# Kernel tuning notes

Hardware: AMD Instinct MI355X
Metric: run time of the kernel (lower is better)

## Reference

```python
import jax, jax.numpy as jnp
import numpy as np

B, T, C, H = 8, 2048, 768, 64

def setup_inputs() -> dict:
    key = jax.random.key(0)
    k1, k2, k3, k4 = jax.random.split(key, 4)
    x = jax.random.normal(k1, (B, T, C), dtype=jnp.float32)
    Wk = jax.random.normal(k2, (C, H), dtype=jnp.float32) * 0.02
    Wq = jax.random.normal(k3, (C, H), dtype=jnp.float32) * 0.02
    Wv = jax.random.normal(k4, (C, H), dtype=jnp.float32) * 0.02
    return {"x": x, "Wk": Wk, "Wq": Wq, "Wv": Wv}

def reference(x, Wk, Wq, Wv):
    # QKV projections (no bias): [B,T,C] @ [C,H] -> [B,T,H]
    k = jnp.einsum('btc,ch->bth', x, Wk)
    q = jnp.einsum('btc,ch->bth', x, Wq)
    v = jnp.einsum('btc,ch->bth', x, Wv)
    scale = 1.0 / jnp.sqrt(jnp.asarray(q.shape[-1], q.dtype))
    # scores: [B,T,T]
    wei = jnp.einsum('bth,bsh->bts', q, k) * scale
    # causal mask: upper triangle (k=1) set to -inf before softmax
    causal = jnp.tril(jnp.ones((wei.shape[1], wei.shape[2]), dtype=bool))
    wei = jnp.where(causal[None, :, :], wei, -jnp.inf)
    wei = jax.nn.softmax(wei, axis=-1)
    # dropout deterministic (training=False) -> identity
    out = jnp.einsum('bts,bsh->bth', wei, v)
    return out
```

## Files before the change

kernel.cpp:

```cpp
#include <hip/hip_runtime.h>
#include <hip/hip_bf16.h>
#include <stdint.h>

#define BB 8
#define TT 2048
#define CC 768
#define NTPB 72

typedef __bf16 bf16x8 __attribute__((ext_vector_type(8)));
typedef float f32x4 __attribute__((ext_vector_type(4)));
typedef float f32x16 __attribute__((ext_vector_type(16)));

__device__ inline __bf16 f2b(float f) {
    __hip_bfloat16 h = __float2bfloat16(f);
    return __builtin_bit_cast(__bf16, h);
}
__device__ inline ushort f2bits(float f) {
    __hip_bfloat16 h = __float2bfloat16(f);
    return __builtin_bit_cast(ushort, h);
}
__device__ inline float bits2f(ushort u) {
    return __builtin_bit_cast(float, ((uint32_t)u) << 16);
}
__device__ inline uint32_t cvtpk(float lo, float hi) {
    uint32_t r;
    asm("v_cvt_pk_bf16_f32 %0, %1, %2" : "=v"(r) : "v"(lo), "v"(hi));
    return r;
}
__device__ inline void pswap(uint32_t& a, uint32_t& b) {
    asm volatile("v_permlane32_swap_b32 %0, %1" : "+v"(a), "+v"(b));
}

#define GLL16(gp, lp)                                                          \
    __builtin_amdgcn_global_load_lds(                                          \
        (const __attribute__((address_space(1))) unsigned int*)(gp),           \
        (__attribute__((address_space(3))) unsigned int*)(lp), 16, 0, 0)

__launch_bounds__(256)
__global__ void wt_kernel(const float* __restrict__ Wk, const float* __restrict__ Wq,
                          const float* __restrict__ Wv, ushort* __restrict__ WtF) {
    __shared__ float tile[32][65];
    int m  = blockIdx.x / 24;
    int c0 = (blockIdx.x % 24) * 32;
    const float* W = (m == 0) ? Wq : ((m == 1) ? Wk : Wv);
    int tid = threadIdx.x;
    {
        int r   = tid >> 3;
        int col = (tid & 7) * 8;
        float4 v0 = *(const float4*)&W[(size_t)(c0 + r) * 64 + col];
        float4 v1 = *(const float4*)&W[(size_t)(c0 + r) * 64 + col + 4];
        tile[r][col]     = v0.x; tile[r][col + 1] = v0.y;
        tile[r][col + 2] = v0.z; tile[r][col + 3] = v0.w;
        tile[r][col + 4] = v1.x; tile[r][col + 5] = v1.y;
        tile[r][col + 6] = v1.z; tile[r][col + 7] = v1.w;
    }
    __syncthreads();
    int j   = tid >> 2;
    int sub = tid & 3;
    int cc  = sub * 8;
    ushort tmp[8];
#pragma unroll
    for (int e = 0; e < 8; e++) tmp[e] = f2bits(tile[cc + e][j]);
    int kc = c0 >> 5;
    ushort* dst = &WtF[((size_t)kc * 192 + m * 64 + j) * 32 + sub * 8];
    *(uint4*)(dst) = *(uint4*)&tmp[0];
}

__launch_bounds__(256, 3)
__global__ void qkv_kernel(const float* __restrict__ x, const ushort* __restrict__ WtF,
                           ushort* __restrict__ qws, ushort* __restrict__ kws,
                           ushort* __restrict__ vws) {
    __shared__ float  xsA[4][32 * 32];
    __shared__ ushort xsB[3][6144];

    int tid  = threadIdx.x;
    int wid  = tid >> 6;
    int lane = tid & 63;
    int l15  = lane & 15;
    int hi4  = lane >> 4;
    int row0 = blockIdx.x * 32;

    int rA  = tid >> 3;
    int gcA = (tid & 7) ^ (rA & 7);
    const float* gpA = x + (size_t)(row0 + rA) * CC + gcA * 4;

    int PB0 = tid, PB1 = tid + 256, PB2 = tid + 512;
    int LB0 = PB0 ^ ((PB0 >> 3) & 3);
    int LB1 = PB1 ^ ((PB1 >> 3) & 3);
    int LB2 = PB2 ^ ((PB2 >> 3) & 3);

    int PrB[3];
#pragma unroll
    for (int nt = 0; nt < 3; nt++) {
        int Lr = (wid * 48 + nt * 16 + l15) * 4 + hi4;
        PrB[nt] = Lr ^ ((Lr >> 3) & 3);
    }

    f32x4 acc[2][3];
#pragma unroll
    for (int mm = 0; mm < 2; mm++)
#pragma unroll
        for (int nt = 0; nt < 3; nt++) acc[mm][nt] = (f32x4){0.f, 0.f, 0.f, 0.f};

    auto stageA = [&](int t) {
        GLL16(gpA + t * 32, &xsA[t & 3][(size_t)tid * 4]);
    };
    auto stageB = [&](int t) {
        int buf = t % 3;
        const ushort* bsrc = WtF + (size_t)t * 6144;
        GLL16(bsrc + LB0 * 8, &xsB[buf][PB0 * 8]);
        GLL16(bsrc + LB1 * 8, &xsB[buf][PB1 * 8]);
        GLL16(bsrc + LB2 * 8, &xsB[buf][PB2 * 8]);
    };

    stageA(0); stageA(1);
    stageB(0); stageB(1);
    stageA(2); stageA(3);

#pragma unroll
    for (int p = 0; p < 12; p++) {
        if (p < 11) asm volatile("s_waitcnt vmcnt(2)" ::: "memory");
        else        asm volatile("s_waitcnt vmcnt(0)" ::: "memory");
        __builtin_amdgcn_s_barrier();
        __builtin_amdgcn_sched_barrier(0);

#pragma unroll
        for (int u = 0; u < 2; u++) {
            int t    = 2 * p + u;
            int bufA = t & 3;
            int bufB = t % 3;
            bf16x8 af[2];
#pragma unroll
            for (int mm = 0; mm < 2; mm++) {
                int row = mm * 16 + l15;
                const float* base = &xsA[bufA][row * 32];
                float4 fa = *(const float4*)(base + (((2 * hi4)     ^ (row & 7)) * 4));
                float4 fb = *(const float4*)(base + (((2 * hi4 + 1) ^ (row & 7)) * 4));
                uint32_t w0 = cvtpk(fa.x, fa.y), w1 = cvtpk(fa.z, fa.w);
                uint32_t w2 = cvtpk(fb.x, fb.y), w3 = cvtpk(fb.z, fb.w);
                uint4 u4 = {w0, w1, w2, w3};
                af[mm] = __builtin_bit_cast(bf16x8, u4);
            }
#pragma unroll
            for (int nt = 0; nt < 3; nt++) {
                bf16x8 b = __builtin_bit_cast(bf16x8, *(const uint4*)&xsB[bufB][PrB[nt] * 8]);
                acc[0][nt] = __builtin_amdgcn_mfma_f32_16x16x32_bf16(af[0], b, acc[0][nt], 0, 0, 0);
                acc[1][nt] = __builtin_amdgcn_mfma_f32_16x16x32_bf16(af[1], b, acc[1][nt], 0, 0, 0);
            }
        }
        __builtin_amdgcn_s_barrier();
        if (p < 11) { stageB(2 * p + 2); stageB(2 * p + 3); }
        if (p < 10) { stageA(2 * p + 4); stageA(2 * p + 5); }
    }

    const float qscale = 0.125f * 1.4426950408889634f;
    int bidx = row0 >> 11;
#pragma unroll
    for (int mm = 0; mm < 2; mm++) {
        int r0 = row0 + mm * 16 + 4 * hi4;
        int t0 = r0 & 2047;
#pragma unroll
        for (int nt = 0; nt < 3; nt++) {
            int c = wid * 48 + nt * 16 + l15;
            int m = c >> 6;
            int j = c & 63;
            if (m == 0) {
#pragma unroll
                for (int r = 0; r < 4; r++)
                    qws[(size_t)(r0 + r) * 64 + j] = f2bits(acc[mm][nt][r] * qscale);
            } else if (m == 1) {
#pragma unroll
                for (int r = 0; r < 4; r++)
                    kws[(size_t)(r0 + r) * 64 + j] = f2bits(acc[mm][nt][r]);
            } else {
                ushort4 pk;
                pk.x = f2bits(acc[mm][nt][0]);
                pk.y = f2bits(acc[mm][nt][1]);
                pk.z = f2bits(acc[mm][nt][2]);
                pk.w = f2bits(acc[mm][nt][3]);
                *(ushort4*)&vws[((size_t)bidx * 64 + j) * TT + t0] = pk;
            }
        }
    }
}

__launch_bounds__(256, 3)
__global__ void flash_kernel(const ushort* __restrict__ qg, const ushort* __restrict__ kg,
                             const ushort* __restrict__ vtg, float* __restrict__ out,
                             ushort* __restrict__ pO, float* __restrict__ pM,
                             float* __restrict__ pL) {
    __shared__ ushort Ks[3][64 * 64];
    __shared__ ushort Vs[3][64 * 64];

    int tid  = threadIdx.x;
    int wid  = tid >> 6;
    int lane = tid & 63;
    int l31  = lane & 31;
    int hi   = lane >> 5;

    int b  = blockIdx.x & 7;
    int tp = blockIdx.x >> 3;
    int g  = 0;
    while (tp >= ((g + 2) * (g + 2)) >> 2) g++;
    int seg   = tp - (((g + 1) * (g + 1)) >> 2);
    int nseg  = (g + 2) >> 1;
    int Qb    = g * 128;
    int Q0w   = Qb + wid * 32;
    int s_beg = seg * 256;
    int s_end = (s_beg + 256 < Qb + 128) ? s_beg + 256 : Qb + 128;
    int nt    = (s_end - s_beg) >> 6;

    int rS  = tid >> 3;
    int gcS = (tid & 7) ^ (rS & 7);
    const ushort* kS = kg  + ((size_t)b * TT + rS) * 64 + gcS * 8;
    const ushort* vS = vtg + ((size_t)b * 64 + rS) * TT + gcS * 8;

    auto stage = [&](int tt) {
        int buf = tt % 3;
        int ss  = s_beg + tt * 64;
        const ushort* kA = kS + (size_t)ss * 64;
        const ushort* vA = vS + ss;
        GLL16(kA,            &Ks[buf][tid * 8]);
        GLL16(kA + 32 * 64,  &Ks[buf][(tid + 256) * 8]);
        GLL16(vA,            &Vs[buf][tid * 8]);
        GLL16(vA + 32 * TT,  &Vs[buf][(tid + 256) * 8]);
    };

    const ushort* qp = qg + ((size_t)b * TT + Q0w + l31) * 64 + hi * 8;
    bf16x8 qf[4];
#pragma unroll
    for (int c = 0; c < 4; c++)
        qf[c] = __builtin_bit_cast(bf16x8, *(const uint4*)(qp + c * 16));

    f32x16 o0 = (f32x16)(0.f), o1 = (f32x16)(0.f);
    float m  = -INFINITY;
    float lp = 0.f;

    stage(0);
    if (nt > 1) stage(1);

    for (int t = 0; t < nt; t++) {
        if (t < nt - 1) asm volatile("s_waitcnt vmcnt(4)" ::: "memory");
        else            asm volatile("s_waitcnt vmcnt(0)" ::: "memory");
        __builtin_amdgcn_s_barrier();
        __builtin_amdgcn_sched_barrier(0);
        if (t + 2 < nt) stage(t + 2);

        int s0 = s_beg + t * 64;
        if (s0 < Q0w + 32) {
            int buf = t % 3;
            bf16x8 kf[2][4];
#pragma unroll
            for (int tt = 0; tt < 2; tt++) {
                int rk = tt * 32 + l31;
                const ushort* base = &Ks[buf][rk * 64];
                int sw = rk & 7;
#pragma unroll
                for (int c = 0; c < 4; c++)
                    kf[tt][c] = __builtin_bit_cast(bf16x8,
                        *(const uint4*)(base + (((c * 2 + hi) ^ sw) * 8)));
            }

            f32x16 st0 = (f32x16)(0.f), st1 = (f32x16)(0.f);
            __builtin_amdgcn_s_setprio(1);
#pragma unroll
            for (int c = 0; c < 4; c++)
                st0 = __builtin_amdgcn_mfma_f32_32x32x16_bf16(kf[0][c], qf[c], st0, 0, 0, 0);
#pragma unroll
            for (int c = 0; c < 4; c++)
                st1 = __builtin_amdgcn_mfma_f32_32x32x16_bf16(kf[1][c], qf[c], st1, 0, 0, 0);
            __builtin_amdgcn_s_setprio(0);

            if (s0 + 63 > Q0w) {
                int th0 = Q0w + l31 - s0 - 4 * hi;
                int th1 = th0 - 32;
#pragma unroll
                for (int r = 0; r < 16; r++) {
                    int kvl = (r & 3) + 8 * (r >> 2);
                    if (kvl > th0) st0[r] = -INFINITY;
                    if (kvl > th1) st1[r] = -INFINITY;
                }
            }

            float a[16];
#pragma unroll
            for (int r = 0; r < 16; r++) a[r] = fmaxf(st0[r], st1[r]);
#pragma unroll
            for (int off = 8; off > 0; off >>= 1)
#pragma unroll
                for (int i = 0; i < 8; i++)
                    if (i < off) a[i] = fmaxf(a[i], a[i + off]);
            float pmax = fmaxf(a[0], __shfl_xor(a[0], 32));
            if (__any(pmax > m + 11.54f)) {
                float mn = fmaxf(m, pmax);
                float al = exp2f(m - mn);
                lp *= al;
#pragma unroll
                for (int r = 0; r < 16; r++) { o0[r] *= al; o1[r] *= al; }
                m = mn;
            }
#pragma unroll
            for (int r = 0; r < 16; r++) {
                st0[r] = exp2f(st0[r] - m);
                st1[r] = exp2f(st1[r] - m);
            }
            float s[16];
#pragma unroll
            for (int r = 0; r < 16; r++) s[r] = st0[r] + st1[r];
#pragma unroll
            for (int off = 8; off > 0; off >>= 1)
#pragma unroll
                for (int i = 0; i < 8; i++)
                    if (i < off) s[i] += s[i + off];
            lp += s[0];

            bf16x8 pf[4];
            {
                uint32_t w0, w1, w2, w3;
                w0 = cvtpk(st0[0], st0[1]);  w1 = cvtpk(st0[2], st0[3]);
                w2 = cvtpk(st0[4], st0[5]);  w3 = cvtpk(st0[6], st0[7]);
                pswap(w0, w2); pswap(w1, w3);
                uint4 u0 = {w0, w1, w2, w3}; pf[0] = __builtin_bit_cast(bf16x8, u0);
                w0 = cvtpk(st0[8], st0[9]);  w1 = cvtpk(st0[10], st0[11]);
                w2 = cvtpk(st0[12], st0[13]); w3 = cvtpk(st0[14], st0[15]);
                pswap(w0, w2); pswap(w1, w3);
                uint4 u1 = {w0, w1, w2, w3}; pf[1] = __builtin_bit_cast(bf16x8, u1);
                w0 = cvtpk(st1[0], st1[1]);  w1 = cvtpk(st1[2], st1[3]);
                w2 = cvtpk(st1[4], st1[5]);  w3 = cvtpk(st1[6], st1[7]);
                pswap(w0, w2); pswap(w1, w3);
                uint4 u2 = {w0, w1, w2, w3}; pf[2] = __builtin_bit_cast(bf16x8, u2);
                w0 = cvtpk(st1[8], st1[9]);  w1 = cvtpk(st1[10], st1[11]);
                w2 = cvtpk(st1[12], st1[13]); w3 = cvtpk(st1[14], st1[15]);
                pswap(w0, w2); pswap(w1, w3);
                uint4 u3 = {w0, w1, w2, w3}; pf[3] = __builtin_bit_cast(bf16x8, u3);
            }

            bf16x8 vf[2][4];
#pragma unroll
            for (int ht = 0; ht < 2; ht++) {
                int rv = ht * 32 + l31;
                const ushort* base = &Vs[buf][rv * 64];
                int sw = rv & 7;
#pragma unroll
                for (int c = 0; c < 4; c++)
                    vf[ht][c] = __builtin_bit_cast(bf16x8,
                        *(const uint4*)(base + (((c * 2 + hi) ^ sw) * 8)));
            }

            __builtin_amdgcn_s_setprio(1);
#pragma unroll
            for (int c = 0; c < 4; c++)
                o0 = __builtin_amdgcn_mfma_f32_32x32x16_bf16(vf[0][c], pf[c], o0, 0, 0, 0);
#pragma unroll
            for (int c = 0; c < 4; c++)
                o1 = __builtin_amdgcn_mfma_f32_32x32x16_bf16(vf[1][c], pf[c], o1, 0, 0, 0);
            __builtin_amdgcn_s_setprio(0);
        }
    }

    float lsum = lp + __shfl_xor(lp, 32);

    if (nseg == 1) {
        float inv = 1.f / lsum;
        float* ob = out + ((size_t)b * TT + Q0w + l31) * 64;
#pragma unroll
        for (int gg = 0; gg < 4; gg++) {
            float4 v0 = {o0[4*gg] * inv, o0[4*gg+1] * inv, o0[4*gg+2] * inv, o0[4*gg+3] * inv};
            *(float4*)(ob + 8 * gg + 4 * hi) = v0;
            float4 v1 = {o1[4*gg] * inv, o1[4*gg+1] * inv, o1[4*gg+2] * inv, o1[4*gg+3] * inv};
            *(float4*)(ob + 32 + 8 * gg + 4 * hi) = v1;
        }
    } else {
        int tb = b * NTPB + tp;
        ushort* pb = pO + (size_t)tb * 8192 + (size_t)(wid * 32 + l31) * 64;
#pragma unroll
        for (int gg = 0; gg < 4; gg++) {
            ushort4 v0 = {f2bits(o0[4*gg]), f2bits(o0[4*gg+1]),
                          f2bits(o0[4*gg+2]), f2bits(o0[4*gg+3])};
            *(ushort4*)(pb + 8 * gg + 4 * hi) = v0;
            ushort4 v1 = {f2bits(o1[4*gg]), f2bits(o1[4*gg+1]),
                          f2bits(o1[4*gg+2]), f2bits(o1[4*gg+3])};
            *(ushort4*)(pb + 32 + 8 * gg + 4 * hi) = v1;
        }
        if (hi == 0) {
            pM[(size_t)tb * 128 + wid * 32 + l31] = m;
            pL[(size_t)tb * 128 + wid * 32 + l31] = lsum;
        }
    }
}

__launch_bounds__(256)
__global__ void merge_kernel(const ushort* __restrict__ pO, const float* __restrict__ pM,
                             const float* __restrict__ pL, float* __restrict__ out) {
    int b    = blockIdx.x / 56;
    int rem  = blockIdx.x % 56;
    int g    = 2 + (rem >> 2);
    int q4   = rem & 3;
    int nseg = (g + 2) >> 1;
    int tbase = b * NTPB + (((g + 1) * (g + 1)) >> 2);

    int row  = q4 * 32 + (threadIdx.x >> 3);
    int colg = (threadIdx.x & 7) * 8;

    float mstar = -INFINITY;
    for (int s = 0; s < nseg; s++)
        mstar = fmaxf(mstar, pM[(size_t)(tbase + s) * 128 + row]);

    float oa[8] = {0.f, 0.f, 0.f, 0.f, 0.f, 0.f, 0.f, 0.f};
    float la = 0.f;
    for (int s = 0; s < nseg; s++) {
        float w = exp2f(pM[(size_t)(tbase + s) * 128 + row] - mstar);
        la += w * pL[(size_t)(tbase + s) * 128 + row];
        uint4 u = *(const uint4*)&pO[(size_t)(tbase + s) * 8192 + (size_t)row * 64 + colg];
#pragma unroll
        for (int e = 0; e < 4; e++) {
            uint32_t wdw = ((const uint32_t*)&u)[e];
            oa[e*2]     += w * bits2f((ushort)(wdw & 0xffff));
            oa[e*2 + 1] += w * bits2f((ushort)(wdw >> 16));
        }
    }
    float inv = 1.f / la;
    float* ob = out + ((size_t)b * TT + g * 128 + row) * 64 + colg;
    float4 r0 = {oa[0] * inv, oa[1] * inv, oa[2] * inv, oa[3] * inv};
    float4 r1 = {oa[4] * inv, oa[5] * inv, oa[6] * inv, oa[7] * inv};
    *(float4*)(ob)     = r0;
    *(float4*)(ob + 4) = r1;
}

extern "C" void kernel_launch(void* const* d_in, const int* in_sizes, int n_in,
                              void* d_out, int out_size, void* d_ws, size_t ws_size,
                              hipStream_t stream) {
    const float* x  = (const float*)d_in[0];
    const float* Wk = (const float*)d_in[1];
    const float* Wq = (const float*)d_in[2];
    const float* Wv = (const float*)d_in[3];
    float* out = (float*)d_out;

    char* ws = (char*)d_ws;
    ushort* WtF = (ushort*)(ws);
    ushort* qws = (ushort*)(ws + 0x50000);
    ushort* kws = (ushort*)(ws + 0x250000);
    ushort* vws = (ushort*)(ws + 0x450000);
    ushort* pO  = (ushort*)(ws + 0x650000);
    float*  pM  = (float*)(ws + 0x1050000);
    float*  pL  = (float*)(ws + 0x1098000);

    wt_kernel<<<72, 256, 0, stream>>>(Wk, Wq, Wv, WtF);
    qkv_kernel<<<(BB * TT) / 32, 256, 0, stream>>>(x, WtF, qws, kws, vws);
    flash_kernel<<<BB * NTPB, 256, 0, stream>>>(qws, kws, vws, out, pO, pM, pL);
    merge_kernel<<<BB * 14 * 4, 256, 0, stream>>>(pO, pM, pL, out);
}
```

Measured before the change: 45.85 us.

## Split flash attention into 128-key segments for more blocks and higher occupancy

Shortens each flash block's KV segment from up to 256 keys to exactly 128 (two 64-key tiles), which raises the block count from 72 to 136 per batch. With the fixed two-tile loop the ring buffer shrinks from three LDS stages to two, and launch bounds are raised to 4 blocks per CU. The merge kernel is remapped to combine more partial segments per query group, starting from group 1 instead of 2. This trades more partial-output traffic and merge work for more parallelism and better load balance in the causal triangle.

```diff
diff --git a/kernel.cpp b/kernel.cpp
--- a/kernel.cpp
+++ b/kernel.cpp
@@ -5,7 +5,7 @@
 #define BB 8
 #define TT 2048
 #define CC 768
-#define NTPB 72
+#define NTPB 136
 
 typedef __bf16 bf16x8 __attribute__((ext_vector_type(8)));
 typedef float f32x4 __attribute__((ext_vector_type(4)));
@@ -184,13 +184,13 @@
     }
 }
 
-__launch_bounds__(256, 3)
+__launch_bounds__(256, 4)
 __global__ void flash_kernel(const ushort* __restrict__ qg, const ushort* __restrict__ kg,
                              const ushort* __restrict__ vtg, float* __restrict__ out,
                              ushort* __restrict__ pO, float* __restrict__ pM,
                              float* __restrict__ pL) {
-    __shared__ ushort Ks[3][64 * 64];
-    __shared__ ushort Vs[3][64 * 64];
+    __shared__ ushort Ks[2][64 * 64];
+    __shared__ ushort Vs[2][64 * 64];
 
     int tid  = threadIdx.x;
     int wid  = tid >> 6;
@@ -201,14 +201,12 @@
     int b  = blockIdx.x & 7;
     int tp = blockIdx.x >> 3;
     int g  = 0;
-    while (tp >= ((g + 2) * (g + 2)) >> 2) g++;
-    int seg   = tp - (((g + 1) * (g + 1)) >> 2);
-    int nseg  = (g + 2) >> 1;
+    while (tp >= ((g + 1) * (g + 2)) >> 1) g++;
+    int seg   = tp - ((g * (g + 1)) >> 1);
+    int nseg  = g + 1;
     int Qb    = g * 128;
     int Q0w   = Qb + wid * 32;
-    int s_beg = seg * 256;
-    int s_end = (s_beg + 256 < Qb + 128) ? s_beg + 256 : Qb + 128;
-    int nt    = (s_end - s_beg) >> 6;
+    int s_beg = seg * 128;
 
     int rS  = tid >> 3;
     int gcS = (tid & 7) ^ (rS & 7);
@@ -216,14 +214,13 @@
     const ushort* vS = vtg + ((size_t)b * 64 + rS) * TT + gcS * 8;
 
     auto stage = [&](int tt) {
-        int buf = tt % 3;
         int ss  = s_beg + tt * 64;
         const ushort* kA = kS + (size_t)ss * 64;
         const ushort* vA = vS + ss;
-        GLL16(kA,            &Ks[buf][tid * 8]);
-        GLL16(kA + 32 * 64,  &Ks[buf][(tid + 256) * 8]);
-        GLL16(vA,            &Vs[buf][tid * 8]);
-        GLL16(vA + 32 * TT,  &Vs[buf][(tid + 256) * 8]);
+        GLL16(kA,            &Ks[tt][tid * 8]);
+        GLL16(kA + 32 * 64,  &Ks[tt][(tid + 256) * 8]);
+        GLL16(vA,            &Vs[tt][tid * 8]);
+        GLL16(vA + 32 * TT,  &Vs[tt][(tid + 256) * 8]);
     };
 
     const ushort* qp = qg + ((size_t)b * TT + Q0w + l31) * 64 + hi * 8;
@@ -237,23 +234,22 @@
     float lp = 0.f;
 
     stage(0);
-    if (nt > 1) stage(1);
-
-    for (int t = 0; t < nt; t++) {
-        if (t < nt - 1) asm volatile("s_waitcnt vmcnt(4)" ::: "memory");
-        else            asm volatile("s_waitcnt vmcnt(0)" ::: "memory");
+    stage(1);
+
+#pragma unroll
+    for (int t = 0; t < 2; t++) {
+        if (t == 0) asm volatile("s_waitcnt vmcnt(4)" ::: "memory");
+        else        asm volatile("s_waitcnt vmcnt(0)" ::: "memory");
         __builtin_amdgcn_s_barrier();
         __builtin_amdgcn_sched_barrier(0);
-        if (t + 2 < nt) stage(t + 2);
 
         int s0 = s_beg + t * 64;
         if (s0 < Q0w + 32) {
-            int buf = t % 3;
             bf16x8 kf[2][4];
 #pragma unroll
             for (int tt = 0; tt < 2; tt++) {
                 int rk = tt * 32 + l31;
-                const ushort* base = &Ks[buf][rk * 64];
+                const ushort* base = &Ks[t][rk * 64];
                 int sw = rk & 7;
 #pragma unroll
                 for (int c = 0; c < 4; c++)
@@ -339,7 +335,7 @@
 #pragma unroll
             for (int ht = 0; ht < 2; ht++) {
                 int rv = ht * 32 + l31;
-                const ushort* base = &Vs[buf][rv * 64];
+                const ushort* base = &Vs[t][rv * 64];
                 int sw = rv & 7;
 #pragma unroll
                 for (int c = 0; c < 4; c++)
@@ -392,12 +388,12 @@
 __launch_bounds__(256)
 __global__ void merge_kernel(const ushort* __restrict__ pO, const float* __restrict__ pM,
                              const float* __restrict__ pL, float* __restrict__ out) {
-    int b    = blockIdx.x / 56;
-    int rem  = blockIdx.x % 56;
-    int g    = 2 + (rem >> 2);
+    int b    = blockIdx.x & 7;
+    int rem  = blockIdx.x >> 3;
+    int g    = 1 + (rem >> 2);
     int q4   = rem & 3;
-    int nseg = (g + 2) >> 1;
-    int tbase = b * NTPB + (((g + 1) * (g + 1)) >> 2);
+    int nseg = g + 1;
+    int tbase = b * NTPB + ((g * (g + 1)) >> 1);
 
     int row  = q4 * 32 + (threadIdx.x >> 3);
     int colg = (threadIdx.x & 7) * 8;
@@ -442,11 +438,11 @@
     ushort* kws = (ushort*)(ws + 0x250000);
     ushort* vws = (ushort*)(ws + 0x450000);
     ushort* pO  = (ushort*)(ws + 0x650000);
-    float*  pM  = (float*)(ws + 0x1050000);
-    float*  pL  = (float*)(ws + 0x1098000);
+    float*  pM  = (float*)(ws + 0x1750000);
+    float*  pL  = (float*)(ws + 0x17D8000);
 
     wt_kernel<<<72, 256, 0, stream>>>(Wk, Wq, Wv, WtF);
     qkv_kernel<<<(BB * TT) / 32, 256, 0, stream>>>(x, WtF, qws, kws, vws);
     flash_kernel<<<BB * NTPB, 256, 0, stream>>>(qws, kws, vws, out, pO, pM, pL);
-    merge_kernel<<<BB * 14 * 4, 256, 0, stream>>>(pO, pM, pL, out);
-}
+    merge_kernel<<<8 * 15 * 4, 256, 0, stream>>>(pO, pM, pL, out);
+}
```

Measured after the change: 49.19 us. +7.3%, slower.
